# Performance work log

Measured on AMD Instinct MI355X. Metric: run time of the kernel, lower is better.

Reference implementation:

```python
import jax, jax.numpy as jnp
import numpy as np

B, T, D_IN, H, NC = 256, 512, 40, 128, 7


def _lstm_dir(x, W_ih, W_hh, b):
    # x: [B,T,D]; W_ih: [4H,D]; W_hh: [4H,H]; b: [4H] (b_ih+b_hh combined)
    pre = jnp.einsum('btd,gd->btg', x, W_ih) + b  # [B,T,4H]
    h0 = jnp.zeros((x.shape[0], W_hh.shape[1]), x.dtype)
    c0 = jnp.zeros_like(h0)

    def step(carry, p_t):
        h, c = carry
        g = p_t + h @ W_hh.T  # [B,4H]
        i, f, gg, o = jnp.split(g, 4, axis=-1)  # PyTorch gate order: i,f,g,o
        i = jax.nn.sigmoid(i)
        f = jax.nn.sigmoid(f)
        gg = jnp.tanh(gg)
        o = jax.nn.sigmoid(o)
        c = f * c + i * gg
        h = o * jnp.tanh(c)
        return (h, c), h

    _, hs = jax.lax.scan(step, (h0, c0), jnp.swapaxes(pre, 0, 1))  # [T,B,H]
    return jnp.swapaxes(hs, 0, 1)  # [B,T,H]


def _bilstm_layer(x, Wf, Uf, bf, Wr, Ur, br):
    fwd = _lstm_dir(x, Wf, Uf, bf)
    rev = _lstm_dir(x[:, ::-1], Wr, Ur, br)[:, ::-1]
    return jnp.concatenate([fwd, rev], axis=-1)  # [B,T,2H]


def setup_inputs() -> dict:
    key = jax.random.key(0)
    ks = jax.random.split(key, 20)
    s = 1.0 / np.sqrt(H)  # PyTorch LSTM init scale

    def u(k, shape):
        return jax.random.uniform(k, shape, jnp.float32, -s, s)

    inp = {
        'x': jax.random.normal(ks[0], (B, T, D_IN), jnp.float32),
        # layer 0 (input dim 40)
        'W_ih_l0_f': u(ks[1], (4 * H, D_IN)), 'W_hh_l0_f': u(ks[2], (4 * H, H)), 'b_l0_f': u(ks[3], (4 * H,)),
        'W_ih_l0_r': u(ks[4], (4 * H, D_IN)), 'W_hh_l0_r': u(ks[5], (4 * H, H)), 'b_l0_r': u(ks[6], (4 * H,)),
        # layer 1 (input dim 2H)
        'W_ih_l1_f': u(ks[7], (4 * H, 2 * H)), 'W_hh_l1_f': u(ks[8], (4 * H, H)), 'b_l1_f': u(ks[9], (4 * H,)),
        'W_ih_l1_r': u(ks[10], (4 * H, 2 * H)), 'W_hh_l1_r': u(ks[11], (4 * H, H)), 'b_l1_r': u(ks[12], (4 * H,)),
        # classifier head
        'fc_w': u(ks[13], (NC, 2 * H)), 'fc_b': u(ks[14], (NC,)),
    }
    return inp


def reference(x, W_ih_l0_f, W_hh_l0_f, b_l0_f, W_ih_l0_r, W_hh_l0_r, b_l0_r,
              W_ih_l1_f, W_hh_l1_f, b_l1_f, W_ih_l1_r, W_hh_l1_r, b_l1_r,
              fc_w, fc_b):
    h1 = _bilstm_layer(x, W_ih_l0_f, W_hh_l0_f, b_l0_f, W_ih_l0_r, W_hh_l0_r, b_l0_r)
    h2 = _bilstm_layer(h1, W_ih_l1_f, W_hh_l1_f, b_l1_f, W_ih_l1_r, W_hh_l1_r, b_l1_r)
    last = h2[:, -1, :]  # [B,2H]; dropout is identity at eval time
    return last @ fc_w.T + fc_b  # [B,NC]
```

## Files before the change

### kernel.cpp

```cpp
#include <hip/hip_runtime.h>
#include <hip/hip_bf16.h>

typedef short short8 __attribute__((ext_vector_type(8)));
typedef short short4v __attribute__((ext_vector_type(4)));
typedef float f32x4 __attribute__((ext_vector_type(4)));
typedef float f32x2 __attribute__((ext_vector_type(2)));
typedef __bf16 bf16x8 __attribute__((ext_vector_type(8)));

#define DEVI static __device__ __forceinline__

#if __has_builtin(__builtin_amdgcn_exp2f)
#define EXP2(x) __builtin_amdgcn_exp2f(x)
#else
#define EXP2(x) exp2f(x)
#endif
#if __has_builtin(__builtin_amdgcn_rcpf)
#define RCP(x) __builtin_amdgcn_rcpf(x)
#else
#define RCP(x) (1.0f / (x))
#endif

static constexpr int BB = 256, TT = 512, DIN0 = 40, HH = 128, NCLS = 7;
static constexpr float L2E = 1.44269504088896f;

DEVI short f2b(float x) {
  union { __hip_bfloat16 h; short s; } u;
  u.h = __float2bfloat16(x);
  return u.s;
}
DEVI float b2f(short s) {
  union { unsigned u; float f; } v;
  v.u = ((unsigned)(unsigned short)s) << 16;
  return v.f;
}
DEVI bf16x8 as_bf(short8 s) { return __builtin_bit_cast(bf16x8, s); }

DEVI void bar_lgkm() {
  asm volatile("s_waitcnt lgkmcnt(0)\n\ts_barrier" ::: "memory");
}

DEVI void cell2(float gi0, float gf0, float gg0, float go0,
                float gi1, float gf1, float gg1, float go1,
                float& c0, float& c1, float& h0, float& h1) {
  float d0 = 1.f + EXP2(fminf(gi0, 14.f));
  float d1 = 1.f + EXP2(fminf(gf0, 14.f));
  float d2 = 1.f + EXP2(fminf(gg0, 14.f));
  float d3 = 1.f + EXP2(fminf(go0, 14.f));
  float d4 = 1.f + EXP2(fminf(gi1, 14.f));
  float d5 = 1.f + EXP2(fminf(gf1, 14.f));
  float d6 = 1.f + EXP2(fminf(gg1, 14.f));
  float d7 = 1.f + EXP2(fminf(go1, 14.f));
  float p1 = d0 * d1, p2 = p1 * d2, p3 = p2 * d3, p4 = p3 * d4;
  float p5 = p4 * d5, p6 = p5 * d6, p7 = p6 * d7;
  float R = RCP(p7);
  float r7 = R * p6; R *= d7;
  float r6 = R * p5; R *= d6;
  float r5 = R * p4; R *= d5;
  float r4 = R * p3; R *= d4;
  float r3 = R * p2; R *= d3;
  float r2 = R * p1; R *= d2;
  float r1 = R * d0, r0 = R * d1;
  float tg0 = 1.f - 2.f * r2, tg1 = 1.f - 2.f * r6;
  c0 = r1 * c0 + r0 * tg0;
  c1 = r5 * c1 + r4 * tg1;
  float q0 = 1.f + EXP2(fminf(c0 * (2.f * L2E), 30.f));
  float q1 = 1.f + EXP2(fminf(c1 * (2.f * L2E), 30.f));
  float Rq = RCP(q0 * q1);
  h0 = r3 * (1.f - 2.f * Rq * q1);
  h1 = r7 * (1.f - 2.f * Rq * q0);
}

__global__ __launch_bounds__(512) void rec0c(
    const float* __restrict__ x0,
    const float* __restrict__ WihF, const float* __restrict__ WhhF,
    const float* __restrict__ bF, const float* __restrict__ WihR,
    const float* __restrict__ WhhR, const float* __restrict__ bR,
    short* __restrict__ h1_out) {
  __shared__ short Hb[2][16][16][8];
  __shared__ short X2[2][8][16][8];

  const int tid = threadIdx.x, w = tid >> 6, lane = tid & 63;
  const int lg = lane >> 4, bcol = lane & 15;
  const int hi = bcol >> 3, col = bcol & 7;
  const int dir = blockIdx.x & 1, b0 = (blockIdx.x >> 1) * 8;
  const int j0 = w * 16 + lg * 4, j0c = j0 + 2 * hi;
  const float* __restrict__ Wih = dir ? WihR : WihF;
  const float* __restrict__ Whh = dir ? WhhR : WhhF;
  const float* __restrict__ bias = dir ? bR : bF;
  auto tmap = [&](int s) { return dir ? (TT - 1 - s) : s; };

  short8 wx[4][2], wh[4][4];
  f32x4 bq[4];
#pragma unroll
  for (int q = 0; q < 4; ++q) {
    const float scale = (q == 2) ? (2.0f * L2E) : (-L2E);
    const int m = q * HH + w * 16 + bcol;
#pragma unroll
    for (int kk = 0; kk < 2; ++kk) {
      short8 f;
#pragma unroll
      for (int e = 0; e < 8; ++e) {
        const int k = kk * 32 + lg * 8 + e;
        float v = (k < DIN0) ? Wih[(size_t)m * DIN0 + k] : 0.0f;
        f[e] = f2b(v * scale);
      }
      wx[q][kk] = f;
    }
#pragma unroll
    for (int kk = 0; kk < 4; ++kk) {
      short8 f;
#pragma unroll
      for (int e = 0; e < 8; ++e)
        f[e] = f2b(Whh[(size_t)m * HH + kk * 32 + lg * 8 + e] * scale);
      wh[q][kk] = f;
    }
#pragma unroll
    for (int r = 0; r < 4; ++r) bq[q][r] = bias[q * HH + j0 + r] * scale;
  }

  for (int i = tid; i < (int)(sizeof(Hb) + sizeof(X2)) / 4; i += 512)
    ((int*)&Hb[0][0][0][0])[i] = 0;
  __syncthreads();

  auto load_x = [&](int s) -> f32x4 {
    f32x4 v = {0.f, 0.f, 0.f, 0.f};
    if (tid < 80) {
      int ss = (s < TT) ? s : (TT - 1);
      v = *(const f32x4*)(x0 + ((size_t)(b0 + tid / 10) * TT + tmap(ss)) * DIN0 + (tid % 10) * 4);
    }
    return v;
  };
  auto stage_x = [&](int buf, const f32x4& v) {
    if (tid < 80) {
      short4v o;
      o[0] = f2b(v[0]); o[1] = f2b(v[1]); o[2] = f2b(v[2]); o[3] = f2b(v[3]);
      const int row = tid / 10, c4 = tid % 10;
      *(short4v*)&X2[buf][c4 >> 1][row][(c4 & 1) * 4] = o;
    }
  };
  auto prefill = [&](f32x4* acc, int p) {
#pragma unroll
    for (int kk = 0; kk < 2; ++kk) {
      const bf16x8 bx = as_bf(*(const short8*)&X2[p][kk * 4 + lg][bcol][0]);
#pragma unroll
      for (int q = 0; q < 4; ++q)
        acc[q] = __builtin_amdgcn_mfma_f32_16x16x32_bf16(
            as_bf(wx[q][kk]), bx, (kk == 0) ? bq[q] : acc[q], 0, 0, 0);
    }
  };

  stage_x(0, load_x(0));
  stage_x(1, load_x(1));
  f32x4 xst = load_x(2);
  __syncthreads();
  f32x4 accA[4], accB[4];
  prefill(accA, 0);
  bar_lgkm();

  float cst0 = 0.f, cst1 = 0.f;

  auto stepf = [&](int s, int cur, f32x4* acc, f32x4* accN) {
#pragma unroll
    for (int kk = 0; kk < 4; ++kk) {
      const bf16x8 bh = as_bf(*(const short8*)&Hb[cur][kk * 4 + lg][bcol][0]);
#pragma unroll
      for (int q = 0; q < 4; ++q)
        acc[q] = __builtin_amdgcn_mfma_f32_16x16x32_bf16(as_bf(wh[q][kk]), bh, acc[q], 0, 0, 0);
    }
    float g[4][2];
#pragma unroll
    for (int q = 0; q < 4; ++q) {
#pragma unroll
      for (int u = 0; u < 2; ++u) {
        float t = __shfl_xor(acc[q][2 + u], 8);
        g[q][u] = hi ? t : acc[q][u];
      }
    }
    float hv0, hv1;
    cell2(g[0][0], g[1][0], g[2][0], g[3][0],
          g[0][1], g[1][1], g[2][1], g[3][1], cst0, cst1, hv0, hv1);
    int pk = (int)(unsigned short)f2b(hv0) | ((int)(unsigned short)f2b(hv1) << 16);
    *(int*)&Hb[cur ^ 1][j0 >> 3][col][(j0 & 7) + 2 * hi] = pk;
    *(int*)(h1_out + (((size_t)(b0 + col) * TT + tmap(s)) << 8) + dir * HH + j0c) = pk;
    stage_x(cur, xst);
    xst = load_x(s + 3);
    prefill(accN, cur ^ 1);
    bar_lgkm();
  };
  for (int s = 0; s < TT; s += 2) {
    stepf(s, 0, accA, accB);
    stepf(s + 1, 1, accB, accA);
  }
}

__global__ __launch_bounds__(512, 1) void pre1(
    const short* __restrict__ h1, const float* __restrict__ WihF,
    const float* __restrict__ bF, const float* __restrict__ WihR,
    const float* __restrict__ bR, short* __restrict__ pre, int cs, int clen) {
  __shared__ short X[16 * 256];
  const int tid = threadIdx.x, w = tid >> 6, lane = tid & 63;
  const int lg = lane >> 4, bcol = lane & 15;
  const int gid = blockIdx.x;
  const int dir = gid & 1, bt16 = (gid >> 1) & 15, tc = gid >> 5;
  const float* __restrict__ Wih = dir ? WihR : WihF;
  const float* __restrict__ bias = dir ? bR : bF;
  const int b0 = bt16 * 16;

  short8 wx[4][8];
  f32x4 bq[4];
#pragma unroll
  for (int q = 0; q < 4; ++q) {
    const float scale = (q == 2) ? (2.0f * L2E) : (-L2E);
    const int m = q * HH + w * 16 + bcol;
#pragma unroll
    for (int kk = 0; kk < 8; ++kk) {
      short8 f;
#pragma unroll
      for (int e = 0; e < 8; ++e)
        f[e] = f2b(Wih[(size_t)m * 256 + kk * 32 + lg * 8 + e] * scale);
      wx[q][kk] = f;
    }
#pragma unroll
    for (int r = 0; r < 4; ++r) bq[q][r] = bias[q * HH + w * 16 + lg * 4 + r] * scale;
  }

  const int srow = tid >> 5, sch = tid & 31;
  for (int i = 0; i < 8; ++i) {
    const int sl = tc * 8 + i, sG = cs + sl;
    const int t = dir ? (TT - 1 - sG) : sG;
    short8 v = *(const short8*)(h1 + (((size_t)(b0 + srow) * TT + t) << 8) + sch * 8);
    *(short8*)((char*)X + srow * 512 + ((sch * 16) ^ ((srow & 7) << 4))) = v;
    __syncthreads();
    f32x4 acc[4] = {bq[0], bq[1], bq[2], bq[3]};
#pragma unroll
    for (int kk = 0; kk < 8; ++kk) {
      const bf16x8 bx = as_bf(*(const short8*)((const char*)X + bcol * 512 +
                                               ((kk * 64 + lg * 16) ^ ((bcol & 7) << 4))));
#pragma unroll
      for (int q = 0; q < 4; ++q)
        acc[q] = __builtin_amdgcn_mfma_f32_16x16x32_bf16(as_bf(wx[q][kk]), bx, acc[q], 0, 0, 0);
    }
    short* op = pre + ((((size_t)dir * 16 + bt16) * clen + sl) * 8 + w) * 1024 + bcol * 16 + lg * 4;
#pragma unroll
    for (int q = 0; q < 4; ++q) {
      short4v o;
      o[0] = f2b(acc[q][0]); o[1] = f2b(acc[q][1]);
      o[2] = f2b(acc[q][2]); o[3] = f2b(acc[q][3]);
      *(short4v*)(op + q * 256) = o;
    }
    __syncthreads();
  }
}

__global__ __launch_bounds__(512) void rec1c(
    const short* __restrict__ pre, const float* __restrict__ WhhF,
    const float* __restrict__ WhhR, float* __restrict__ h2last,
    float* __restrict__ cstate, int* __restrict__ hstate, int cs, int clen) {
  __shared__ short Hb[2][16][16][8];
  const int tid = threadIdx.x, w = tid >> 6, lane = tid & 63;
  const int lg = lane >> 4, bcol = lane & 15;
  const int hi = bcol >> 3, col = bcol & 7;
  const int dir = blockIdx.x & 1, bt8 = blockIdx.x >> 1;
  const int b0 = bt8 * 8, bt16 = bt8 >> 1, half = bt8 & 1;
  const int j0 = w * 16 + lg * 4, j0c = j0 + 2 * hi;
  const int wg = blockIdx.x;
  const float* __restrict__ Whh = dir ? WhhR : WhhF;

  short8 wh[4][4];
#pragma unroll
  for (int q = 0; q < 4; ++q) {
    const float scale = (q == 2) ? (2.0f * L2E) : (-L2E);
    const int m = q * HH + w * 16 + bcol;
#pragma unroll
    for (int kk = 0; kk < 4; ++kk) {
      short8 f;
#pragma unroll
      for (int e = 0; e < 8; ++e)
        f[e] = f2b(Whh[(size_t)m * HH + kk * 32 + lg * 8 + e] * scale);
      wh[q][kk] = f;
    }
  }
  for (int i = tid; i < (int)sizeof(Hb) / 4; i += 512) ((int*)&Hb[0][0][0][0])[i] = 0;
  __syncthreads();

  float cst0 = 0.f, cst1 = 0.f;
  int pkLast = 0;
  if (cs != 0) {
    cst0 = cstate[(wg * 512 + tid) * 2];
    cst1 = cstate[(wg * 512 + tid) * 2 + 1];
    pkLast = hstate[wg * 512 + tid];
    *(int*)&Hb[0][j0 >> 3][col][(j0 & 7) + 2 * hi] = pkLast;
  }
  __syncthreads();

  const int col16 = half * 8 + col;
  auto ldpre = [&](short4v* dst, int ls) {
    int l = (ls < clen) ? ls : (clen - 1);
    const short* bp = pre + ((((size_t)dir * 16 + bt16) * clen + l) * 8 + w) * 1024 +
                      col16 * 16 + lg * 4;
#pragma unroll
    for (int q = 0; q < 4; ++q) dst[q] = *(const short4v*)(bp + q * 256);
  };

  short4v pA[4], pB[4];
  ldpre(pA, 0);
  ldpre(pB, 1);

  auto stepf = [&](int ls, int cur, short4v* P) {
    f32x4 acc[4];
#pragma unroll
    for (int q = 0; q < 4; ++q)
#pragma unroll
      for (int r = 0; r < 4; ++r) acc[q][r] = b2f(P[q][r]);
#pragma unroll
    for (int kk = 0; kk < 4; ++kk) {
      const bf16x8 bh = as_bf(*(const short8*)&Hb[cur][kk * 4 + lg][bcol][0]);
#pragma unroll
      for (int q = 0; q < 4; ++q)
        acc[q] = __builtin_amdgcn_mfma_f32_16x16x32_bf16(as_bf(wh[q][kk]), bh, acc[q], 0, 0, 0);
    }
    float g[4][2];
#pragma unroll
    for (int q = 0; q < 4; ++q) {
#pragma unroll
      for (int u = 0; u < 2; ++u) {
        float t = __shfl_xor(acc[q][2 + u], 8);
        g[q][u] = hi ? t : acc[q][u];
      }
    }
    float hv0, hv1;
    cell2(g[0][0], g[1][0], g[2][0], g[3][0],
          g[0][1], g[1][1], g[2][1], g[3][1], cst0, cst1, hv0, hv1);
    int pk = (int)(unsigned short)f2b(hv0) | ((int)(unsigned short)f2b(hv1) << 16);
    pkLast = pk;
    *(int*)&Hb[cur ^ 1][j0 >> 3][col][(j0 & 7) + 2 * hi] = pk;
    const int sG = cs + ls;
    if (sG == (dir ? 0 : TT - 1)) {
      f32x2 o;
      o[0] = hv0; o[1] = hv1;
      *(f32x2*)(h2last + ((size_t)(b0 + col) << 8) + dir * HH + j0c) = o;
    }
    ldpre(P, ls + 2);
    bar_lgkm();
  };
  for (int ls = 0; ls < clen; ls += 2) {
    stepf(ls, 0, pA);
    stepf(ls + 1, 1, pB);
  }
  cstate[(wg * 512 + tid) * 2] = cst0;
  cstate[(wg * 512 + tid) * 2 + 1] = cst1;
  hstate[wg * 512 + tid] = pkLast;
}

__global__ __launch_bounds__(512) void rec1_fused(
    const short* __restrict__ h1, const float* __restrict__ Wih_f,
    const float* __restrict__ Whh_f, const float* __restrict__ b_f,
    const float* __restrict__ Wih_r, const float* __restrict__ Whh_r,
    const float* __restrict__ b_r, float* __restrict__ h2last) {
  __shared__ short Hb[2][16][16][8];
  __shared__ char Xraw[16384];
  const int tid = threadIdx.x, w = tid >> 6, lane = tid & 63;
  const int lg = lane >> 4, bcol = lane & 15;
  const int dir = blockIdx.x & 1, b0 = (blockIdx.x >> 1) * 16;
  const int j0 = w * 16 + lg * 4;
  const float* __restrict__ Wih = dir ? Wih_r : Wih_f;
  const float* __restrict__ Whh = dir ? Whh_r : Whh_f;
  const float* __restrict__ bias = dir ? b_r : b_f;
  auto tmap = [&](int s) { return dir ? (TT - 1 - s) : s; };

  short8 wx[4][8], wh[4][4];
  f32x4 bq[4];
#pragma unroll
  for (int q = 0; q < 4; ++q) {
    const float scale = (q == 2) ? (2.0f * L2E) : (-L2E);
    const int m = q * HH + w * 16 + bcol;
#pragma unroll
    for (int kk = 0; kk < 8; ++kk) {
      short8 f;
#pragma unroll
      for (int e = 0; e < 8; ++e)
        f[e] = f2b(Wih[(size_t)m * 256 + kk * 32 + lg * 8 + e] * scale);
      wx[q][kk] = f;
    }
#pragma unroll
    for (int kk = 0; kk < 4; ++kk) {
      short8 f;
#pragma unroll
      for (int e = 0; e < 8; ++e)
        f[e] = f2b(Whh[(size_t)m * HH + kk * 32 + lg * 8 + e] * scale);
      wh[q][kk] = f;
    }
#pragma unroll
    for (int r = 0; r < 4; ++r) bq[q][r] = bias[q * HH + j0 + r] * scale;
  }
  for (int i = tid; i < 2 * 16 * 16 * 4; i += 512) ((int*)Hb)[i] = 0;
  __syncthreads();

  const int xr1 = tid >> 5;
  const int xcb = ((tid << 4) ^ (((tid >> 5) & 7) << 4)) & 511;
  auto ldx = [&](int p, int kk) -> short8 {
    int byte = ((bcol << 9) + (kk << 6) + (lg << 4)) ^ ((bcol & 7) << 4);
    return *(const short8*)(Xraw + p * 8192 + byte);
  };
  auto ldg = [&](int s) -> short8 {
    int ss = (s < TT) ? s : (TT - 1);
    return *(const short8*)((const char*)h1 + (((size_t)(b0 + xr1) * TT + tmap(ss)) << 9) + xcb);
  };
  {
    short8 v0 = ldg(0), v1 = ldg(1);
    *(short8*)(Xraw + tid * 16) = v0;
    *(short8*)(Xraw + 8192 + tid * 16) = v1;
  }
  short8 xstage = ldg(2);
  __syncthreads();

  f32x4 acc[4] = {bq[0], bq[1], bq[2], bq[3]};
#pragma unroll
  for (int kk = 0; kk < 8; ++kk) {
    bf16x8 bx = as_bf(ldx(0, kk));
#pragma unroll
    for (int q = 0; q < 4; ++q)
      acc[q] = __builtin_amdgcn_mfma_f32_16x16x32_bf16(as_bf(wx[q][kk]), bx, acc[q], 0, 0, 0);
  }
  bar_lgkm();

  f32x4 cst = {0.f, 0.f, 0.f, 0.f};
  auto stepf = [&](int s, int buf) {
    *(short8*)(Xraw + buf * 8192 + tid * 16) = xstage;
    xstage = ldg(s + 3);
#pragma unroll
    for (int kk = 0; kk < 4; ++kk) {
      bf16x8 bh = as_bf(*(const short8*)&Hb[buf][kk * 4 + lg][bcol][0]);
#pragma unroll
      for (int q = 0; q < 4; ++q)
        acc[q] = __builtin_amdgcn_mfma_f32_16x16x32_bf16(as_bf(wh[q][kk]), bh, acc[q], 0, 0, 0);
    }
    float hv0, hv1, hv2, hv3;
    {
      float c0 = cst[0], c1 = cst[1];
      cell2(acc[0][0], acc[1][0], acc[2][0], acc[3][0],
            acc[0][1], acc[1][1], acc[2][1], acc[3][1], c0, c1, hv0, hv1);
      cst[0] = c0; cst[1] = c1;
      float c2 = cst[2], c3 = cst[3];
      cell2(acc[0][2], acc[1][2], acc[2][2], acc[3][2],
            acc[0][3], acc[1][3], acc[2][3], acc[3][3], c2, c3, hv2, hv3);
      cst[2] = c2; cst[3] = c3;
    }
    short4v hp;
    hp[0] = f2b(hv0); hp[1] = f2b(hv1); hp[2] = f2b(hv2); hp[3] = f2b(hv3);
    *(short4v*)&Hb[buf ^ 1][j0 >> 3][bcol][j0 & 7] = hp;
    if ((dir == 0 && s == TT - 1) || (dir == 1 && s == 0)) {
      f32x4 hf;
      hf[0] = hv0; hf[1] = hv1; hf[2] = hv2; hf[3] = hv3;
      *(f32x4*)(h2last + ((size_t)(b0 + bcol) << 8) + dir * HH + j0) = hf;
    }
#pragma unroll
    for (int q = 0; q < 4; ++q) acc[q] = bq[q];
#pragma unroll
    for (int kk = 0; kk < 8; ++kk) {
      bf16x8 bx = as_bf(ldx(buf ^ 1, kk));
#pragma unroll
      for (int q = 0; q < 4; ++q)
        acc[q] = __builtin_amdgcn_mfma_f32_16x16x32_bf16(as_bf(wx[q][kk]), bx, acc[q], 0, 0, 0);
    }
    bar_lgkm();
  };
  for (int s = 0; s < TT; s += 2) {
    stepf(s, 0);
    stepf(s + 1, 1);
  }
}

__global__ void fc_kernel(const float* __restrict__ h2last,
                          const float* __restrict__ fcw,
                          const float* __restrict__ fcb,
                          float* __restrict__ out) {
  const int gid = blockIdx.x * blockDim.x + threadIdx.x;
  if (gid >= BB * NCLS) return;
  const int b = gid / NCLS, n = gid % NCLS;
  const float* hp = h2last + (size_t)b * 256;
  const float* wp = fcw + (size_t)n * 256;
  float s = fcb[n];
#pragma unroll 8
  for (int j = 0; j < 256; ++j) s = fmaf(hp[j], wp[j], s);
  out[gid] = s;
}

extern "C" void kernel_launch(void* const* d_in, const int* in_sizes, int n_in,
                              void* d_out, int out_size, void* d_ws, size_t ws_size,
                              hipStream_t stream) {
  const float* x     = (const float*)d_in[0];
  const float* Wih0f = (const float*)d_in[1];
  const float* Whh0f = (const float*)d_in[2];
  const float* b0f   = (const float*)d_in[3];
  const float* Wih0r = (const float*)d_in[4];
  const float* Whh0r = (const float*)d_in[5];
  const float* b0r   = (const float*)d_in[6];
  const float* Wih1f = (const float*)d_in[7];
  const float* Whh1f = (const float*)d_in[8];
  const float* b1f   = (const float*)d_in[9];
  const float* Wih1r = (const float*)d_in[10];
  const float* Whh1r = (const float*)d_in[11];
  const float* b1r   = (const float*)d_in[12];
  const float* fcw   = (const float*)d_in[13];
  const float* fcb   = (const float*)d_in[14];

  short* h1 = (short*)d_ws;
  float* h2last = (float*)((char*)d_ws + (64ull << 20));
  float* cstate = (float*)((char*)d_ws + (64ull << 20) + (512ull << 10));
  int* hstate = (int*)((char*)d_ws + (64ull << 20) + (768ull << 10));
  short* pre = (short*)((char*)d_ws + (66ull << 20));

  size_t budget = ws_size > (66ull << 20) ? ws_size - (66ull << 20) : 0;
  int chunkT = 0;
  const int cands[7] = {512, 256, 128, 64, 32, 16, 8};
  for (int i = 0; i < 7; ++i)
    if ((size_t)cands[i] * (512ull << 10) <= budget) { chunkT = cands[i]; break; }

  rec0c<<<dim3(64), dim3(512), 0, stream>>>(
      x, Wih0f, Whh0f, b0f, Wih0r, Whh0r, b0r, h1);

  if (chunkT > 0) {
    for (int cs = 0; cs < TT; cs += chunkT) {
      pre1<<<dim3(4 * chunkT), dim3(512), 0, stream>>>(
          h1, Wih1f, b1f, Wih1r, b1r, pre, cs, chunkT);
      rec1c<<<dim3(64), dim3(512), 0, stream>>>(
          pre, Whh1f, Whh1r, h2last, cstate, hstate, cs, chunkT);
    }
  } else {
    rec1_fused<<<dim3(32), dim3(512), 0, stream>>>(
        h1, Wih1f, Whh1f, b1f, Wih1r, Whh1r, b1r, h2last);
  }

  fc_kernel<<<dim3((BB * NCLS + 255) / 256), dim3(256), 0, stream>>>(
      h2last, fcw, fcb, (float*)d_out);
}
```

Baseline: 1.042 ms.

## Interleave two independent batch groups per block in both recurrent LSTM kernels

Each block of the layer-0 and layer-1 recurrence kernels now handles two independent 8-sequence batch groups (P and Q). Their timesteps are interleaved so that the MFMA, shuffle and transcendental latency of one group can overlap with the other. This halves the grid from 64 to 32 blocks and shares one barrier between the two groups per step. In exchange it doubles per-block registers and LDS, leaves more CUs idle, and makes each block do twice the serial work.

```diff
diff --git a/kernel.cpp b/kernel.cpp
--- a/kernel.cpp
+++ b/kernel.cpp
@@ -70,19 +70,20 @@
   h1 = r7 * (1.f - 2.f * Rq * q0);
 }
 
-__global__ __launch_bounds__(512) void rec0c(
+__global__ __launch_bounds__(512) void rec0i(
     const float* __restrict__ x0,
     const float* __restrict__ WihF, const float* __restrict__ WhhF,
     const float* __restrict__ bF, const float* __restrict__ WihR,
     const float* __restrict__ WhhR, const float* __restrict__ bR,
     short* __restrict__ h1_out) {
-  __shared__ short Hb[2][16][16][8];
-  __shared__ short X2[2][8][16][8];
+  __shared__ short HbP[2][16][16][8], HbQ[2][16][16][8];
+  __shared__ short XP[2][8][16][8], XQ[2][8][16][8];
 
   const int tid = threadIdx.x, w = tid >> 6, lane = tid & 63;
   const int lg = lane >> 4, bcol = lane & 15;
   const int hi = bcol >> 3, col = bcol & 7;
-  const int dir = blockIdx.x & 1, b0 = (blockIdx.x >> 1) * 8;
+  const int dir = blockIdx.x & 1;
+  const int b0P = (blockIdx.x >> 1) * 16, b0Q = b0P + 8;
   const int j0 = w * 16 + lg * 4, j0c = j0 + 2 * hi;
   const float* __restrict__ Wih = dir ? WihR : WihF;
   const float* __restrict__ Whh = dir ? WhhR : WhhF;
@@ -118,11 +119,17 @@
     for (int r = 0; r < 4; ++r) bq[q][r] = bias[q * HH + j0 + r] * scale;
   }
 
-  for (int i = tid; i < (int)(sizeof(Hb) + sizeof(X2)) / 4; i += 512)
-    ((int*)&Hb[0][0][0][0])[i] = 0;
+  for (int i = tid; i < 2 * 16 * 16 * 4; i += 512) {
+    ((int*)HbP)[i] = 0;
+    ((int*)HbQ)[i] = 0;
+  }
+  for (int i = tid; i < 2 * 8 * 16 * 4; i += 512) {
+    ((int*)XP)[i] = 0;
+    ((int*)XQ)[i] = 0;
+  }
   __syncthreads();
 
-  auto load_x = [&](int s) -> f32x4 {
+  auto load_x = [&](int b0, int s) -> f32x4 {
     f32x4 v = {0.f, 0.f, 0.f, 0.f};
     if (tid < 80) {
       int ss = (s < TT) ? s : (TT - 1);
@@ -130,7 +137,7 @@
     }
     return v;
   };
-  auto stage_x = [&](int buf, const f32x4& v) {
+  auto stage_x = [&](short (&X2)[2][8][16][8], int buf, const f32x4& v) {
     if (tid < 80) {
       short4v o;
       o[0] = f2b(v[0]); o[1] = f2b(v[1]); o[2] = f2b(v[2]); o[3] = f2b(v[3]);
@@ -138,7 +145,7 @@
       *(short4v*)&X2[buf][c4 >> 1][row][(c4 & 1) * 4] = o;
     }
   };
-  auto prefill = [&](f32x4* acc, int p) {
+  auto prefill = [&](f32x4* acc, short (&X2)[2][8][16][8], int p) {
 #pragma unroll
     for (int kk = 0; kk < 2; ++kk) {
       const bf16x8 bx = as_bf(*(const short8*)&X2[p][kk * 4 + lg][bcol][0]);
@@ -149,17 +156,9 @@
     }
   };
 
-  stage_x(0, load_x(0));
-  stage_x(1, load_x(1));
-  f32x4 xst = load_x(2);
-  __syncthreads();
-  f32x4 accA[4], accB[4];
-  prefill(accA, 0);
-  bar_lgkm();
-
-  float cst0 = 0.f, cst1 = 0.f;
-
-  auto stepf = [&](int s, int cur, f32x4* acc, f32x4* accN) {
+  auto tstep = [&](int s, int cur, short (&Hb)[2][16][16][8],
+                   short (&X2)[2][8][16][8], f32x4* acc, f32x4* accN,
+                   float& c0s, float& c1s, f32x4& xst, int b0) {
 #pragma unroll
     for (int kk = 0; kk < 4; ++kk) {
       const bf16x8 bh = as_bf(*(const short8*)&Hb[cur][kk * 4 + lg][bcol][0]);
@@ -178,18 +177,36 @@
     }
     float hv0, hv1;
     cell2(g[0][0], g[1][0], g[2][0], g[3][0],
-          g[0][1], g[1][1], g[2][1], g[3][1], cst0, cst1, hv0, hv1);
+          g[0][1], g[1][1], g[2][1], g[3][1], c0s, c1s, hv0, hv1);
     int pk = (int)(unsigned short)f2b(hv0) | ((int)(unsigned short)f2b(hv1) << 16);
     *(int*)&Hb[cur ^ 1][j0 >> 3][col][(j0 & 7) + 2 * hi] = pk;
     *(int*)(h1_out + (((size_t)(b0 + col) * TT + tmap(s)) << 8) + dir * HH + j0c) = pk;
-    stage_x(cur, xst);
-    xst = load_x(s + 3);
-    prefill(accN, cur ^ 1);
+    stage_x(X2, cur, xst);
+    xst = load_x(b0, s + 3);
+    prefill(accN, X2, cur ^ 1);
+  };
+
+  stage_x(XP, 0, load_x(b0P, 0));
+  stage_x(XP, 1, load_x(b0P, 1));
+  f32x4 xstP = load_x(b0P, 2);
+  stage_x(XQ, 0, load_x(b0Q, 0));
+  stage_x(XQ, 1, load_x(b0Q, 1));
+  f32x4 xstQ = load_x(b0Q, 2);
+  __syncthreads();
+  f32x4 accAP[4], accBP[4], accAQ[4], accBQ[4];
+  prefill(accAP, XP, 0);
+  prefill(accAQ, XQ, 0);
+  bar_lgkm();
+
+  float c0P = 0.f, c1P = 0.f, c0Q = 0.f, c1Q = 0.f;
+
+  for (int s = 0; s < TT; s += 2) {
+    tstep(s, 0, HbP, XP, accAP, accBP, c0P, c1P, xstP, b0P);
+    tstep(s, 0, HbQ, XQ, accAQ, accBQ, c0Q, c1Q, xstQ, b0Q);
     bar_lgkm();
-  };
-  for (int s = 0; s < TT; s += 2) {
-    stepf(s, 0, accA, accB);
-    stepf(s + 1, 1, accB, accA);
+    tstep(s + 1, 1, HbP, XP, accBP, accAP, c0P, c1P, xstP, b0P);
+    tstep(s + 1, 1, HbQ, XQ, accBQ, accAQ, c0Q, c1Q, xstQ, b0Q);
+    bar_lgkm();
   }
 }
 
@@ -252,18 +269,18 @@
   }
 }
 
-__global__ __launch_bounds__(512) void rec1c(
+__global__ __launch_bounds__(512) void rec1i(
     const short* __restrict__ pre, const float* __restrict__ WhhF,
     const float* __restrict__ WhhR, float* __restrict__ h2last,
     float* __restrict__ cstate, int* __restrict__ hstate, int cs, int clen) {
-  __shared__ short Hb[2][16][16][8];
+  __shared__ short HbP[2][16][16][8], HbQ[2][16][16][8];
   const int tid = threadIdx.x, w = tid >> 6, lane = tid & 63;
   const int lg = lane >> 4, bcol = lane & 15;
   const int hi = bcol >> 3, col = bcol & 7;
-  const int dir = blockIdx.x & 1, bt8 = blockIdx.x >> 1;
-  const int b0 = bt8 * 8, bt16 = bt8 >> 1, half = bt8 & 1;
+  const int dir = blockIdx.x & 1, bt16 = blockIdx.x >> 1;
+  const int b0P = bt16 * 16, b0Q = b0P + 8;
+  const int col16P = col, col16Q = col + 8;
   const int j0 = w * 16 + lg * 4, j0c = j0 + 2 * hi;
-  const int wg = blockIdx.x;
   const float* __restrict__ Whh = dir ? WhhR : WhhF;
 
   short8 wh[4][4];
@@ -280,21 +297,25 @@
       wh[q][kk] = f;
     }
   }
-  for (int i = tid; i < (int)sizeof(Hb) / 4; i += 512) ((int*)&Hb[0][0][0][0])[i] = 0;
+  for (int i = tid; i < 2 * 16 * 16 * 4; i += 512) {
+    ((int*)HbP)[i] = 0;
+    ((int*)HbQ)[i] = 0;
+  }
   __syncthreads();
 
-  float cst0 = 0.f, cst1 = 0.f;
-  int pkLast = 0;
+  const int slotP = (blockIdx.x * 2 + 0) * 512 + tid;
+  const int slotQ = (blockIdx.x * 2 + 1) * 512 + tid;
+  float c0P = 0.f, c1P = 0.f, c0Q = 0.f, c1Q = 0.f;
+  int pkP = 0, pkQ = 0;
   if (cs != 0) {
-    cst0 = cstate[(wg * 512 + tid) * 2];
-    cst1 = cstate[(wg * 512 + tid) * 2 + 1];
-    pkLast = hstate[wg * 512 + tid];
-    *(int*)&Hb[0][j0 >> 3][col][(j0 & 7) + 2 * hi] = pkLast;
+    c0P = cstate[slotP * 2]; c1P = cstate[slotP * 2 + 1]; pkP = hstate[slotP];
+    c0Q = cstate[slotQ * 2]; c1Q = cstate[slotQ * 2 + 1]; pkQ = hstate[slotQ];
+    *(int*)&HbP[0][j0 >> 3][col][(j0 & 7) + 2 * hi] = pkP;
+    *(int*)&HbQ[0][j0 >> 3][col][(j0 & 7) + 2 * hi] = pkQ;
   }
   __syncthreads();
 
-  const int col16 = half * 8 + col;
-  auto ldpre = [&](short4v* dst, int ls) {
+  auto ldpre = [&](short4v* dst, int col16, int ls) {
     int l = (ls < clen) ? ls : (clen - 1);
     const short* bp = pre + ((((size_t)dir * 16 + bt16) * clen + l) * 8 + w) * 1024 +
                       col16 * 16 + lg * 4;
@@ -302,11 +323,8 @@
     for (int q = 0; q < 4; ++q) dst[q] = *(const short4v*)(bp + q * 256);
   };
 
-  short4v pA[4], pB[4];
-  ldpre(pA, 0);
-  ldpre(pB, 1);
-
-  auto stepf = [&](int ls, int cur, short4v* P) {
+  auto tstep = [&](int ls, int cur, short (&Hb)[2][16][16][8], short4v* P,
+                   int col16, float& c0s, float& c1s, int& pkLast, int b0) {
     f32x4 acc[4];
 #pragma unroll
     for (int q = 0; q < 4; ++q)
@@ -330,7 +348,7 @@
     }
     float hv0, hv1;
     cell2(g[0][0], g[1][0], g[2][0], g[3][0],
-          g[0][1], g[1][1], g[2][1], g[3][1], cst0, cst1, hv0, hv1);
+          g[0][1], g[1][1], g[2][1], g[3][1], c0s, c1s, hv0, hv1);
     int pk = (int)(unsigned short)f2b(hv0) | ((int)(unsigned short)f2b(hv1) << 16);
     pkLast = pk;
     *(int*)&Hb[cur ^ 1][j0 >> 3][col][(j0 & 7) + 2 * hi] = pk;
@@ -340,16 +358,25 @@
       o[0] = hv0; o[1] = hv1;
       *(f32x2*)(h2last + ((size_t)(b0 + col) << 8) + dir * HH + j0c) = o;
     }
-    ldpre(P, ls + 2);
+    ldpre(P, col16, ls + 2);
+  };
+
+  short4v pAP[4], pBP[4], pAQ[4], pBQ[4];
+  ldpre(pAP, col16P, 0);
+  ldpre(pBP, col16P, 1);
+  ldpre(pAQ, col16Q, 0);
+  ldpre(pBQ, col16Q, 1);
+
+  for (int ls = 0; ls < clen; ls += 2) {
+    tstep(ls, 0, HbP, pAP, col16P, c0P, c1P, pkP, b0P);
+    tstep(ls, 0, HbQ, pAQ, col16Q, c0Q, c1Q, pkQ, b0Q);
     bar_lgkm();
-  };
-  for (int ls = 0; ls < clen; ls += 2) {
-    stepf(ls, 0, pA);
-    stepf(ls + 1, 1, pB);
-  }
-  cstate[(wg * 512 + tid) * 2] = cst0;
-  cstate[(wg * 512 + tid) * 2 + 1] = cst1;
-  hstate[wg * 512 + tid] = pkLast;
+    tstep(ls + 1, 1, HbP, pBP, col16P, c0P, c1P, pkP, b0P);
+    tstep(ls + 1, 1, HbQ, pBQ, col16Q, c0Q, c1Q, pkQ, b0Q);
+    bar_lgkm();
+  }
+  cstate[slotP * 2] = c0P; cstate[slotP * 2 + 1] = c1P; hstate[slotP] = pkP;
+  cstate[slotQ * 2] = c0Q; cstate[slotQ * 2 + 1] = c1Q; hstate[slotQ] = pkQ;
 }
 
 __global__ __launch_bounds__(512) void rec1_fused(
@@ -517,14 +544,14 @@
   for (int i = 0; i < 7; ++i)
     if ((size_t)cands[i] * (512ull << 10) <= budget) { chunkT = cands[i]; break; }
 
-  rec0c<<<dim3(64), dim3(512), 0, stream>>>(
+  rec0i<<<dim3(32), dim3(512), 0, stream>>>(
       x, Wih0f, Whh0f, b0f, Wih0r, Whh0r, b0r, h1);
 
   if (chunkT > 0) {
     for (int cs = 0; cs < TT; cs += chunkT) {
       pre1<<<dim3(4 * chunkT), dim3(512), 0, stream>>>(
           h1, Wih1f, b1f, Wih1r, b1r, pre, cs, chunkT);
-      rec1c<<<dim3(64), dim3(512), 0, stream>>>(
+      rec1i<<<dim3(32), dim3(512), 0, stream>>>(
           pre, Whh1f, Whh1r, h2last, cstate, hstate, cs, chunkT);
     }
   } else {
```

Measured after the change: 1.654 ms. +58.7%, slower.

## Split recurrent kernels to 4 batch rows per block for more workgroups

Applied to the files above, without the earlier changes.

The layer-0 and layer-1 recurrent kernels now handle 4 batch columns per workgroup instead of 8, so twice as many workgroups (128) run the sequential time loop. Each lane computes a single LSTM cell, with a two-stage shuffle compaction and a 4-gate cell routine. The goal is to spread the latency-bound recurrence over more CUs and shorten each step's elementwise tail. In exchange, half of each MFMA's 16 batch columns are wasted, stores become 2-byte scalars, and the weight loads per block are duplicated.

```diff
diff --git a/kernel.cpp b/kernel.cpp
--- a/kernel.cpp
+++ b/kernel.cpp
@@ -4,7 +4,6 @@
 typedef short short8 __attribute__((ext_vector_type(8)));
 typedef short short4v __attribute__((ext_vector_type(4)));
 typedef float f32x4 __attribute__((ext_vector_type(4)));
-typedef float f32x2 __attribute__((ext_vector_type(2)));
 typedef __bf16 bf16x8 __attribute__((ext_vector_type(8)));
 
 #define DEVI static __device__ __forceinline__
@@ -37,6 +36,22 @@
 
 DEVI void bar_lgkm() {
   asm volatile("s_waitcnt lgkmcnt(0)\n\ts_barrier" ::: "memory");
+}
+
+DEVI void cell1(float gi, float gf, float gg, float go, float& c, float& h) {
+  float d0 = 1.f + EXP2(fminf(gi, 14.f));
+  float d1 = 1.f + EXP2(fminf(gf, 14.f));
+  float d2 = 1.f + EXP2(fminf(gg, 14.f));
+  float d3 = 1.f + EXP2(fminf(go, 14.f));
+  float p1 = d0 * d1, p2 = p1 * d2, p3 = p2 * d3;
+  float R = RCP(p3);
+  float r3 = R * p2; R *= d3;
+  float r2 = R * p1; R *= d2;
+  float r1 = R * d0, r0 = R * d1;
+  float tg = 1.f - 2.f * r2;
+  c = r1 * c + r0 * tg;
+  float q0 = 1.f + EXP2(fminf(c * (2.f * L2E), 30.f));
+  h = r3 * (1.f - 2.f * RCP(q0));
 }
 
 DEVI void cell2(float gi0, float gf0, float gg0, float go0,
@@ -70,7 +85,18 @@
   h1 = r7 * (1.f - 2.f * Rq * q0);
 }
 
-__global__ __launch_bounds__(512) void rec0c(
+#define COMPACT4(g, acc, hi2, hi)                       \
+  {                                                     \
+    float s0 = acc[0], s1 = acc[1], s2 = acc[2], s3 = acc[3]; \
+    float t1 = __shfl_xor(s1, 4);                       \
+    float t3 = __shfl_xor(s3, 4);                       \
+    float u0 = hi2 ? t1 : s0;                           \
+    float u2 = hi2 ? t3 : s2;                           \
+    float v2 = __shfl_xor(u2, 8);                       \
+    g = hi ? v2 : u0;                                   \
+  }
+
+__global__ __launch_bounds__(512) void rec0c4(
     const float* __restrict__ x0,
     const float* __restrict__ WihF, const float* __restrict__ WhhF,
     const float* __restrict__ bF, const float* __restrict__ WihR,
@@ -81,9 +107,10 @@
 
   const int tid = threadIdx.x, w = tid >> 6, lane = tid & 63;
   const int lg = lane >> 4, bcol = lane & 15;
-  const int hi = bcol >> 3, col = bcol & 7;
-  const int dir = blockIdx.x & 1, b0 = (blockIdx.x >> 1) * 8;
-  const int j0 = w * 16 + lg * 4, j0c = j0 + 2 * hi;
+  const int hi = (bcol >> 3) & 1, hi2 = (bcol >> 2) & 1;
+  const int rr = bcol >> 2, ccol = bcol & 3;
+  const int dir = blockIdx.x & 1, b0 = (blockIdx.x >> 1) * 4;
+  const int j0 = w * 16 + lg * 4, jj = j0 + rr;
   const float* __restrict__ Wih = dir ? WihR : WihF;
   const float* __restrict__ Whh = dir ? WhhR : WhhF;
   const float* __restrict__ bias = dir ? bR : bF;
@@ -124,14 +151,14 @@
 
   auto load_x = [&](int s) -> f32x4 {
     f32x4 v = {0.f, 0.f, 0.f, 0.f};
-    if (tid < 80) {
+    if (tid < 40) {
       int ss = (s < TT) ? s : (TT - 1);
       v = *(const f32x4*)(x0 + ((size_t)(b0 + tid / 10) * TT + tmap(ss)) * DIN0 + (tid % 10) * 4);
     }
     return v;
   };
   auto stage_x = [&](int buf, const f32x4& v) {
-    if (tid < 80) {
+    if (tid < 40) {
       short4v o;
       o[0] = f2b(v[0]); o[1] = f2b(v[1]); o[2] = f2b(v[2]); o[3] = f2b(v[3]);
       const int row = tid / 10, c4 = tid % 10;
@@ -157,7 +184,7 @@
   prefill(accA, 0);
   bar_lgkm();
 
-  float cst0 = 0.f, cst1 = 0.f;
+  float cst = 0.f;
 
   auto stepf = [&](int s, int cur, f32x4* acc, f32x4* accN) {
 #pragma unroll
@@ -167,21 +194,16 @@
       for (int q = 0; q < 4; ++q)
         acc[q] = __builtin_amdgcn_mfma_f32_16x16x32_bf16(as_bf(wh[q][kk]), bh, acc[q], 0, 0, 0);
     }
-    float g[4][2];
-#pragma unroll
-    for (int q = 0; q < 4; ++q) {
-#pragma unroll
-      for (int u = 0; u < 2; ++u) {
-        float t = __shfl_xor(acc[q][2 + u], 8);
-        g[q][u] = hi ? t : acc[q][u];
-      }
-    }
-    float hv0, hv1;
-    cell2(g[0][0], g[1][0], g[2][0], g[3][0],
-          g[0][1], g[1][1], g[2][1], g[3][1], cst0, cst1, hv0, hv1);
-    int pk = (int)(unsigned short)f2b(hv0) | ((int)(unsigned short)f2b(hv1) << 16);
-    *(int*)&Hb[cur ^ 1][j0 >> 3][col][(j0 & 7) + 2 * hi] = pk;
-    *(int*)(h1_out + (((size_t)(b0 + col) * TT + tmap(s)) << 8) + dir * HH + j0c) = pk;
+    float g0, g1, g2, g3;
+    COMPACT4(g0, acc[0], hi2, hi);
+    COMPACT4(g1, acc[1], hi2, hi);
+    COMPACT4(g2, acc[2], hi2, hi);
+    COMPACT4(g3, acc[3], hi2, hi);
+    float hv;
+    cell1(g0, g1, g2, g3, cst, hv);
+    short hs = f2b(hv);
+    Hb[cur ^ 1][jj >> 3][ccol][jj & 7] = hs;
+    h1_out[(((size_t)(b0 + ccol) * TT + tmap(s)) << 8) + dir * HH + jj] = hs;
     stage_x(cur, xst);
     xst = load_x(s + 3);
     prefill(accN, cur ^ 1);
@@ -252,17 +274,18 @@
   }
 }
 
-__global__ __launch_bounds__(512) void rec1c(
+__global__ __launch_bounds__(512) void rec1c4(
     const short* __restrict__ pre, const float* __restrict__ WhhF,
     const float* __restrict__ WhhR, float* __restrict__ h2last,
     float* __restrict__ cstate, int* __restrict__ hstate, int cs, int clen) {
   __shared__ short Hb[2][16][16][8];
   const int tid = threadIdx.x, w = tid >> 6, lane = tid & 63;
   const int lg = lane >> 4, bcol = lane & 15;
-  const int hi = bcol >> 3, col = bcol & 7;
-  const int dir = blockIdx.x & 1, bt8 = blockIdx.x >> 1;
-  const int b0 = bt8 * 8, bt16 = bt8 >> 1, half = bt8 & 1;
-  const int j0 = w * 16 + lg * 4, j0c = j0 + 2 * hi;
+  const int hi = (bcol >> 3) & 1, hi2 = (bcol >> 2) & 1;
+  const int rr = bcol >> 2, ccol = bcol & 3;
+  const int dir = blockIdx.x & 1, bt4 = blockIdx.x >> 1;
+  const int b0 = bt4 * 4, bt16 = bt4 >> 2, colhi = (bt4 & 3) * 4;
+  const int j0 = w * 16 + lg * 4, jj = j0 + rr;
   const int wg = blockIdx.x;
   const float* __restrict__ Whh = dir ? WhhR : WhhF;
 
@@ -283,21 +306,19 @@
   for (int i = tid; i < (int)sizeof(Hb) / 4; i += 512) ((int*)&Hb[0][0][0][0])[i] = 0;
   __syncthreads();
 
-  float cst0 = 0.f, cst1 = 0.f;
-  int pkLast = 0;
+  float cst = 0.f;
+  short hLast = 0;
   if (cs != 0) {
-    cst0 = cstate[(wg * 512 + tid) * 2];
-    cst1 = cstate[(wg * 512 + tid) * 2 + 1];
-    pkLast = hstate[wg * 512 + tid];
-    *(int*)&Hb[0][j0 >> 3][col][(j0 & 7) + 2 * hi] = pkLast;
+    cst = cstate[wg * 512 + tid];
+    hLast = (short)hstate[wg * 512 + tid];
+    Hb[0][jj >> 3][ccol][jj & 7] = hLast;
   }
   __syncthreads();
 
-  const int col16 = half * 8 + col;
   auto ldpre = [&](short4v* dst, int ls) {
     int l = (ls < clen) ? ls : (clen - 1);
     const short* bp = pre + ((((size_t)dir * 16 + bt16) * clen + l) * 8 + w) * 1024 +
-                      col16 * 16 + lg * 4;
+                      (colhi + ccol) * 16 + lg * 4;
 #pragma unroll
     for (int q = 0; q < 4; ++q) dst[q] = *(const short4v*)(bp + q * 256);
   };
@@ -319,27 +340,19 @@
       for (int q = 0; q < 4; ++q)
         acc[q] = __builtin_amdgcn_mfma_f32_16x16x32_bf16(as_bf(wh[q][kk]), bh, acc[q], 0, 0, 0);
     }
-    float g[4][2];
-#pragma unroll
-    for (int q = 0; q < 4; ++q) {
-#pragma unroll
-      for (int u = 0; u < 2; ++u) {
-        float t = __shfl_xor(acc[q][2 + u], 8);
-        g[q][u] = hi ? t : acc[q][u];
-      }
-    }
-    float hv0, hv1;
-    cell2(g[0][0], g[1][0], g[2][0], g[3][0],
-          g[0][1], g[1][1], g[2][1], g[3][1], cst0, cst1, hv0, hv1);
-    int pk = (int)(unsigned short)f2b(hv0) | ((int)(unsigned short)f2b(hv1) << 16);
-    pkLast = pk;
-    *(int*)&Hb[cur ^ 1][j0 >> 3][col][(j0 & 7) + 2 * hi] = pk;
+    float g0, g1, g2, g3;
+    COMPACT4(g0, acc[0], hi2, hi);
+    COMPACT4(g1, acc[1], hi2, hi);
+    COMPACT4(g2, acc[2], hi2, hi);
+    COMPACT4(g3, acc[3], hi2, hi);
+    float hv;
+    cell1(g0, g1, g2, g3, cst, hv);
+    short hs = f2b(hv);
+    hLast = hs;
+    Hb[cur ^ 1][jj >> 3][ccol][jj & 7] = hs;
     const int sG = cs + ls;
-    if (sG == (dir ? 0 : TT - 1)) {
-      f32x2 o;
-      o[0] = hv0; o[1] = hv1;
-      *(f32x2*)(h2last + ((size_t)(b0 + col) << 8) + dir * HH + j0c) = o;
-    }
+    if (sG == (dir ? 0 : TT - 1))
+      h2last[((size_t)(b0 + ccol) << 8) + dir * HH + jj] = hv;
     ldpre(P, ls + 2);
     bar_lgkm();
   };
@@ -347,9 +360,8 @@
     stepf(ls, 0, pA);
     stepf(ls + 1, 1, pB);
   }
-  cstate[(wg * 512 + tid) * 2] = cst0;
-  cstate[(wg * 512 + tid) * 2 + 1] = cst1;
-  hstate[wg * 512 + tid] = pkLast;
+  cstate[wg * 512 + tid] = cst;
+  hstate[wg * 512 + tid] = (int)hLast;
 }
 
 __global__ __launch_bounds__(512) void rec1_fused(
@@ -517,14 +529,14 @@
   for (int i = 0; i < 7; ++i)
     if ((size_t)cands[i] * (512ull << 10) <= budget) { chunkT = cands[i]; break; }
 
-  rec0c<<<dim3(64), dim3(512), 0, stream>>>(
+  rec0c4<<<dim3(128), dim3(512), 0, stream>>>(
       x, Wih0f, Whh0f, b0f, Wih0r, Whh0r, b0r, h1);
 
   if (chunkT > 0) {
     for (int cs = 0; cs < TT; cs += chunkT) {
       pre1<<<dim3(4 * chunkT), dim3(512), 0, stream>>>(
           h1, Wih1f, b1f, Wih1r, b1r, pre, cs, chunkT);
-      rec1c<<<dim3(64), dim3(512), 0, stream>>>(
+      rec1c4<<<dim3(128), dim3(512), 0, stream>>>(
           pre, Whh1f, Whh1r, h2last, cstate, hstate, cs, chunkT);
     }
   } else {
```

Result: faster. 991.1 us, median of 3 (-4.9%).
